# Performance work log

Hardware: AMD Instinct MI355X
Metric: run time of the kernel (lower is better)

The kernel has to match this reference:

```python
import jax, jax.numpy as jnp
import numpy as np


def _gru_scan(x, m, d, Wih, Whh, bih, bhh):
    # Returns pre-update hidden at each step (hiddens.append(hidden) BEFORE rnn_cell)
    H = Whh.shape[1]
    B = x.shape[0]
    h0 = jnp.zeros((B, H), x.dtype)
    xs = (jnp.swapaxes(x, 0, 1), jnp.swapaxes(m, 0, 1), jnp.swapaxes(d, 0, 1))  # [T,B,V]

    def step(h, inp):
        xt, mt, dt = inp
        gi = jnp.concatenate([xt, mt, dt], axis=1) @ Wih.T + bih  # [B,3H]
        gh = h @ Whh.T + bhh
        ir, iz, inn = jnp.split(gi, 3, axis=1)
        hr, hz, hn = jnp.split(gh, 3, axis=1)
        r = jax.nn.sigmoid(ir + hr)
        z = jax.nn.sigmoid(iz + hz)
        n = jnp.tanh(inn + r * hn)
        h_new = (1.0 - z) * n + z * h
        return h_new, h

    _, hs = jax.lax.scan(step, h0, xs)
    return jnp.swapaxes(hs, 0, 1)  # [B,T,H]


def setup_inputs() -> dict:
    key = jax.random.key(0)
    B, T, V, H = 512, 128, 59, 512
    ks = jax.random.split(key, 12)

    def u(k, shape, fan_in):
        s = 1.0 / np.sqrt(fan_in).astype(np.float32)
        return jax.random.uniform(k, shape, jnp.float32, -s, s)

    return {
        "values": jax.random.normal(ks[0], (B, T, V), jnp.float32),
        "masks": (jax.random.uniform(ks[1], (B, T, V)) < 0.8).astype(jnp.float32),
        "deltas_f": jax.random.uniform(ks[2], (B, T, V), jnp.float32),
        "deltas_b": jax.random.uniform(ks[3], (B, T, V), jnp.float32),
        # GRUCell(input=3V, hidden=H)
        "Wih": u(ks[4], (3 * H, 3 * V), 3 * V),
        "Whh": u(ks[5], (3 * H, H), H),
        "bih": jnp.zeros((3 * H,), jnp.float32),
        "bhh": jnp.zeros((3 * H,), jnp.float32),
        # hist_reg: Linear(2H -> V)
        "Wh": u(ks[6], (V, 2 * H), 2 * H),
        "bh": jnp.zeros((V,), jnp.float32),
        "Wf": u(ks[7], (V, V), V),
        "bf": jnp.zeros((V,), jnp.float32),
        # weight_combine: Linear(2V -> V)
        "Wc": u(ks[8], (V, 2 * V), 2 * V),
        "bc": jnp.zeros((V,), jnp.float32),
        # imputation: Linear(V -> V)
        "Wi": u(ks[9], (V, V), V),
        "bi": jnp.zeros((V,), jnp.float32),
    }


def reference(values, masks, deltas_f, deltas_b, Wih, Whh, bih, bhh,
              Wh, bh, Wf, bf, Wc, bc, Wi, bi):
    V = values.shape[-1]
    # forward-direction hiddens
    hf = _gru_scan(values, masks, deltas_f, Wih, Whh, bih, bhh)  # [B,T,H]
    # backward-direction: run GRU on time-flipped x/masks with deltas_b, then reverse list
    hb = _gru_scan(values[:, ::-1], masks[:, ::-1], deltas_b, Wih, Whh, bih, bhh)[:, ::-1]
    h = jnp.concatenate([hf, hb], axis=-1)  # [B,T,2H]
    x_v = h @ Wh.T + bh  # hist_reg
    mdiag = 1.0 - jnp.eye(V, dtype=values.dtype)
    x_u = values @ (Wf * mdiag).T + bf  # feat_reg
    x_h = x_u + jnp.concatenate([x_v, masks], axis=-1) @ Wc.T + bc
    imp = x_h @ Wi.T + bi
    # per-timestep masked MAE, summed over T (denominator is per-step mask count)
    num = jnp.sum(jnp.abs(values - imp) * masks, axis=(0, 2))  # [T]
    den = jnp.sum(masks, axis=(0, 2)) + 1e-5
    x_loss = jnp.sum(num / den)
    x_imp = masks * values + (1.0 - masks) * imp
    return x_imp, x_loss
```

## Files before the change

kernel.cpp:

```cpp
#include <hip/hip_runtime.h>
#include <stdint.h>


typedef unsigned short ushort_t;
typedef __bf16 bf16x8 __attribute__((ext_vector_type(8)));
typedef float f32x4 __attribute__((ext_vector_type(4)));
typedef unsigned int u32x4 __attribute__((ext_vector_type(4)));

__device__ __forceinline__ ushort_t f2bf(float f) {
    union { float f; uint32_t u; } c; c.f = f;
    uint32_t u = c.u;
    uint32_t r = (u + 0x7FFFu + ((u >> 16) & 1u)) >> 16;
    return (ushort_t)r;
}

__device__ __forceinline__ u32x4 load_b128_cached(const void* p) {
    u32x4 d;
    asm volatile("global_load_dwordx4 %0, %1, off" : "=v"(d) : "v"(p) : "memory");
    return d;
}
__device__ __forceinline__ u32x4 load_b128_mall(const void* p) {
    u32x4 d;
    asm volatile("global_load_dwordx4 %0, %1, off sc0 sc1" : "=v"(d) : "v"(p) : "memory");
    return d;
}
__device__ __forceinline__ void store_b16_mall(void* p, unsigned v) {
    asm volatile("global_store_short %0, %1, off sc0 sc1" :: "v"(p), "v"(v) : "memory");
}

__device__ __forceinline__ float fast_sigmoid(float x) {
    float e = __expf(-x);
    return __builtin_amdgcn_rcpf(1.f + e);
}
__device__ __forceinline__ float fast_tanh(float x) {
    float xc = fminf(fmaxf(x, -15.f), 15.f);
    float e = __expf(-2.f * xc);
    return (1.f - e) * __builtin_amdgcn_rcpf(1.f + e);
}

__global__ void prep_small(const float* __restrict__ Wih, const float* __restrict__ Whh,
                           const float* __restrict__ Wh,
                           const float* __restrict__ Wf, const float* __restrict__ bf_,
                           const float* __restrict__ Wc, const float* __restrict__ bc,
                           const float* __restrict__ Wi, const float* __restrict__ bi,
                           ushort_t* __restrict__ WhhB, ushort_t* __restrict__ WihB,
                           ushort_t* __restrict__ WhpB,
                           ushort_t* __restrict__ hf0, ushort_t* __restrict__ hb0,
                           float* __restrict__ hstate,
                           ushort_t* __restrict__ Wpost1, ushort_t* __restrict__ Wpost2,
                           float* __restrict__ bcP, float* __restrict__ biP,
                           unsigned* __restrict__ bar, float* __restrict__ outp)
{
    long long gid = (long long)blockIdx.x * blockDim.x + threadIdx.x;
    long long stride = (long long)gridDim.x * blockDim.x;

    if (gid == 0) outp[3866624] = 0.f;
    for (long long i = gid; i < 16 * 64; i += stride) bar[i] = 0u;
    for (long long i = gid; i < 1024LL * 512; i += stride) hstate[i] = 0.f;
    for (long long i = gid; i < 512LL * 512; i += stride) { hf0[i] = 0; hb0[i] = 0; }
    for (long long i = gid; i < 1536LL * 512; i += stride) WhhB[i] = f2bf(Whh[i]);
    for (long long i = gid; i < 1536LL * 192; i += stride) {
        int n = (int)(i / 192), c = (int)(i % 192);
        WihB[i] = (c < 177) ? f2bf(Wih[n * 177 + c]) : (ushort_t)0;
    }
    for (long long i = gid; i < 64LL * 1024; i += stride) {
        int n = (int)(i >> 10), k = (int)(i & 1023);
        WhpB[i] = (n < 59) ? f2bf(Wh[n * 1024 + k]) : (ushort_t)0;
    }
    for (long long i = gid; i < 64LL * 192; i += stride) {
        int n = (int)(i / 192), c = (int)(i % 192);
        float w = 0.f;
        if (n < 59) {
            if (c < 59)       w = (c == n) ? 0.f : Wf[n * 59 + c];
            else if (c < 118) w = Wc[n * 118 + (c - 59)];
            else if (c < 177) w = Wc[n * 118 + 59 + (c - 118)];
        }
        Wpost1[i] = f2bf(w);
    }
    for (long long i = gid; i < 64LL * 64; i += stride) {
        int n = (int)(i >> 6), k = (int)(i & 63);
        Wpost2[i] = (n < 59 && k < 59) ? f2bf(Wi[n * 59 + k]) : (ushort_t)0;
    }
    for (long long i = gid; i < 64; i += stride) {
        bcP[i] = (i < 59) ? (bf_[i] + bc[i]) : 0.f;
        biP[i] = (i < 59) ? bi[i] : 0.f;
    }
}

__global__ __launch_bounds__(192)
void prep_panels(const float* __restrict__ values, const float* __restrict__ masks,
                 const float* __restrict__ deltas_f, const float* __restrict__ deltas_b,
                 ushort_t* __restrict__ xcat_f, ushort_t* __restrict__ xcat_b,
                 ushort_t* __restrict__ pcat)
{
    const int row = blockIdx.x;
    const int c = threadIdx.x;
    const int b = row >> 7, t = row & 127;
    const int tr = 127 - t;
    const long long rowr = (long long)b * 128 + tr;

    float vf = 0.f;
    if (c < 59)       vf = values  [(long long)row * 59 + c];
    else if (c < 118) vf = masks   [(long long)row * 59 + (c - 59)];
    else if (c < 177) vf = deltas_f[(long long)row * 59 + (c - 118)];
    xcat_f[((size_t)t * 512 + b) * 192 + c] = (c < 177) ? f2bf(vf) : (ushort_t)0;

    float vb = 0.f;
    if (c < 59)       vb = values  [rowr * 59 + c];
    else if (c < 118) vb = masks   [rowr * 59 + (c - 59)];
    else if (c < 177) vb = deltas_b[(long long)row * 59 + (c - 118)];
    xcat_b[((size_t)t * 512 + b) * 192 + c] = (c < 177) ? f2bf(vb) : (ushort_t)0;

    if (c < 59)
        pcat[(size_t)row * 192 + c] = f2bf(values[(long long)row * 59 + c]);
    else if (c >= 118 && c < 177)
        pcat[(size_t)row * 192 + c] = f2bf(masks[(long long)row * 59 + (c - 118)]);
    else if (c >= 177)
        pcat[(size_t)row * 192 + c] = 0;
}

__global__ __launch_bounds__(512)
void recurrence_kernel(const ushort_t* __restrict__ WhhB, const ushort_t* __restrict__ WihB,
                       const float* __restrict__ bih, const float* __restrict__ bhh,
                       const ushort_t* __restrict__ xcat_f, const ushort_t* __restrict__ xcat_b,
                       ushort_t* __restrict__ hfS, ushort_t* __restrict__ hbS,
                       unsigned* __restrict__ bar)
{
    extern __shared__ char smem_c[];
    ushort_t* Bw = (ushort_t*)smem_c;
    ushort_t* As = Bw + 96 * 704;

    const int tid  = threadIdx.x;
    const int blk  = blockIdx.x;
    const int ublk = blk & 15;
    const int mblk = blk >> 4;
    const int u0   = ublk * 32;
    const bool fwd = (mblk < 8);
    const int rbase = (fwd ? mblk : mblk - 8) * 64;
    const ushort_t* xbase = fwd ? xcat_f : xcat_b;
    ushort_t* hS = fwd ? hfS : hbS;
    unsigned* gctr = bar + (unsigned)mblk * 64;

    for (int i = tid; i < 96 * 88; i += 512) {
        int row = i / 88, q = i - row * 88;
        int g = row >> 5, u = u0 + (row & 31);
        const ushort_t* src = (q < 64)
            ? WhhB + ((size_t)(g * 512 + u)) * 512 + q * 8
            : WihB + ((size_t)(g * 512 + u)) * 192 + (q - 64) * 8;
        int qs = q ^ (row & 7);
        *(u32x4*)&Bw[row * 704 + qs * 8] = *(const u32x4*)src;
    }

    const int lane = tid & 63, wv = tid >> 6;
    const int mt = wv >> 1, tc = wv & 1;
    const int l15 = lane & 15, lhi = lane >> 4;
    const int arow = tid >> 3, aj = tid & 7;
    const int awoff = arow * 64 + ((aj ^ (arow & 7)) * 8);
    const int aSw = l15 & 7;

    const int u = u0 + tc * 16 + l15;
    const float bR  = bih[u] + bhh[u];
    const float bZ  = bih[512 + u] + bhh[512 + u];
    const float bNX = bih[1024 + u];
    const float bNH = bhh[1024 + u];
    asm volatile("" :: "v"(bR), "v"(bZ), "v"(bNX), "v"(bNH));
    asm volatile("s_waitcnt vmcnt(0) lgkmcnt(0)" ::: "memory");
    __syncthreads();

    f32x4 hreg = {0.f, 0.f, 0.f, 0.f};
    f32x4 zero = {0.f, 0.f, 0.f, 0.f};
    u32x4 rx[3];
    u32x4 rh[5];

    auto mfma_pos = [&](int cbuf, int jBbase, f32x4& aR, f32x4& aZ, f32x4& accN) {
        const ushort_t* Ab = As + cbuf * 4096;
        #pragma unroll
        for (int ks = 0; ks < 64; ks += 32) {
            int j  = (ks >> 3) + lhi;
            int jB = jBbase + j;
            bf16x8 a  = *(const bf16x8*)&Ab[(mt * 16 + l15) * 64 + ((j ^ aSw) * 8)];
            bf16x8 b0 = *(const bf16x8*)&Bw[( 0 + tc * 16 + l15) * 704 + ((jB ^ aSw) * 8)];
            bf16x8 b1 = *(const bf16x8*)&Bw[(32 + tc * 16 + l15) * 704 + ((jB ^ aSw) * 8)];
            bf16x8 b2 = *(const bf16x8*)&Bw[(64 + tc * 16 + l15) * 704 + ((jB ^ aSw) * 8)];
            aR   = __builtin_amdgcn_mfma_f32_16x16x32_bf16(a, b0, aR, 0, 0, 0);
            aZ   = __builtin_amdgcn_mfma_f32_16x16x32_bf16(a, b1, aZ, 0, 0, 0);
            accN = __builtin_amdgcn_mfma_f32_16x16x32_bf16(a, b2, accN, 0, 0, 0);
        }
    };

    {
        const ushort_t* xr0 = xbase + (size_t)(rbase + arow) * 192 + aj * 8;
        rx[0] = load_b128_cached(xr0);
        rx[1] = load_b128_cached(xr0 + 64);
        rx[2] = load_b128_cached(xr0 + 128);
    }
    asm volatile("s_waitcnt vmcnt(0)" ::: "memory");

    for (int t = 0; t < 127; ++t) {
        const ushort_t* hrow = hS + (size_t)t * 262144 + (size_t)(rbase + arow) * 512 + aj * 8;
        ushort_t* hdst = hS + (size_t)(t + 1) * 262144;

        f32x4 accR = zero, accZ = zero, accNX = zero, accNH = zero;

        rh[0] = load_b128_mall(hrow);
        rh[1] = load_b128_mall(hrow + 64);
        rh[2] = load_b128_mall(hrow + 128);

        *(u32x4*)&As[awoff] = rx[0];
        __syncthreads();

        mfma_pos(0, 64, accR, accZ, accNX);
        rh[3] = load_b128_mall(hrow + 3 * 64);
        *(u32x4*)&As[4096 + awoff] = rx[1];
        __syncthreads();

        mfma_pos(1, 72, accR, accZ, accNX);
        rh[4] = load_b128_mall(hrow + 4 * 64);
        *(u32x4*)&As[awoff] = rx[2];
        {
            const ushort_t* xrn = xbase + (size_t)(t + 1) * 98304
                                + (size_t)(rbase + arow) * 192 + aj * 8;
            rx[0] = load_b128_cached(xrn);
            rx[1] = load_b128_cached(xrn + 64);
            rx[2] = load_b128_cached(xrn + 128);
        }
        __syncthreads();

        mfma_pos(0, 80, accR, accZ, accNX);
        asm volatile("s_waitcnt vmcnt(7)" ::: "memory");
        *(u32x4*)&As[4096 + awoff] = rh[0];
        rh[0] = load_b128_mall(hrow + 5 * 64);
        __syncthreads();

        mfma_pos(1, 0, accR, accZ, accNH);
        asm volatile("s_waitcnt vmcnt(7)" ::: "memory");
        *(u32x4*)&As[awoff] = rh[1];
        rh[1] = load_b128_mall(hrow + 6 * 64);
        __syncthreads();

        mfma_pos(0, 8, accR, accZ, accNH);
        asm volatile("s_waitcnt vmcnt(7)" ::: "memory");
        *(u32x4*)&As[4096 + awoff] = rh[2];
        rh[2] = load_b128_mall(hrow + 7 * 64);
        __syncthreads();

        mfma_pos(1, 16, accR, accZ, accNH);
        asm volatile("s_waitcnt vmcnt(7)" ::: "memory");
        *(u32x4*)&As[awoff] = rh[3];
        __syncthreads();

        mfma_pos(0, 24, accR, accZ, accNH);
        asm volatile("s_waitcnt vmcnt(6)" ::: "memory");
        *(u32x4*)&As[4096 + awoff] = rh[4];
        __syncthreads();

        mfma_pos(1, 32, accR, accZ, accNH);
        asm volatile("s_waitcnt vmcnt(2)" ::: "memory");
        *(u32x4*)&As[awoff] = rh[0];
        __syncthreads();

        mfma_pos(0, 40, accR, accZ, accNH);
        asm volatile("s_waitcnt vmcnt(1)" ::: "memory");
        *(u32x4*)&As[4096 + awoff] = rh[1];
        __syncthreads();

        mfma_pos(1, 48, accR, accZ, accNH);
        asm volatile("s_waitcnt vmcnt(0)" ::: "memory");
        *(u32x4*)&As[awoff] = rh[2];
        __syncthreads();

        mfma_pos(0, 56, accR, accZ, accNH);

        #pragma unroll
        for (int reg = 0; reg < 4; ++reg) {
            int m = rbase + mt * 16 + lhi * 4 + reg;
            float rr = fast_sigmoid(accR[reg] + bR);
            float zz = fast_sigmoid(accZ[reg] + bZ);
            float nn = fast_tanh(accNX[reg] + bNX + rr * (accNH[reg] + bNH));
            float hnew = (1.f - zz) * nn + zz * hreg[reg];
            hreg[reg] = hnew;
            store_b16_mall(hdst + (size_t)m * 512 + u, (unsigned)f2bf(hnew));
        }

        if (t < 126) {
            asm volatile("s_waitcnt vmcnt(0)" ::: "memory");
            __syncthreads();
            if (tid == 0) {
                atomicAdd(gctr, 1u);
                unsigned target = (unsigned)(t + 1) * 16u;
                while (__hip_atomic_load(gctr, __ATOMIC_RELAXED,
                                         __HIP_MEMORY_SCOPE_AGENT) < target)
                    __builtin_amdgcn_s_sleep(1);
            }
            __syncthreads();
        }
    }
}

__global__ __launch_bounds__(512)
void step_kernel(const ushort_t* __restrict__ hsrcF, const ushort_t* __restrict__ hsrcB,
                 ushort_t* __restrict__ hdstF, ushort_t* __restrict__ hdstB,
                 const ushort_t* __restrict__ xF, const ushort_t* __restrict__ xB,
                 const ushort_t* __restrict__ WhhB, const ushort_t* __restrict__ WihB,
                 const float* __restrict__ bih, const float* __restrict__ bhh,
                 float* __restrict__ hstate)
{
    __shared__ __align__(16) ushort_t As[64 * 64];
    __shared__ __align__(16) ushort_t Bs[96 * 64];

    const int tid  = threadIdx.x;
    const int ublk = blockIdx.x;
    const int mblk = blockIdx.y;
    const int u0   = ublk * 32;
    const bool fwd = (mblk < 8);
    const ushort_t* hsrc = fwd ? hsrcF : hsrcB;
    const ushort_t* xsrc = fwd ? xF : xB;
    ushort_t* hdst = fwd ? hdstF : hdstB;
    const int rbase = (fwd ? mblk : mblk - 8) * 64;

    const int lane = tid & 63, wv = tid >> 6;
    const int mt = wv >> 1, tc = wv & 1;
    const int l15 = lane & 15, lhi = lane >> 4;

    f32x4 zero = {0.f, 0.f, 0.f, 0.f};
    f32x4 accR = zero, accZ = zero, accNH = zero, accNX = zero;
    const int arow = tid >> 3, ac8 = (tid & 7) * 8;

    for (int chunk = 0; chunk < 11; ++chunk) {
        const bool ph1 = (chunk < 8);
        {
            const ushort_t* src = ph1
                ? hsrc + ((size_t)(rbase + arow)) * 512 + chunk * 64 + ac8
                : xsrc + ((size_t)(rbase + arow)) * 192 + (chunk - 8) * 64 + ac8;
            *(uint4*)&As[arow * 64 + ac8] = *(const uint4*)src;
        }
        {
            int rowB = tid >> 3; int c8 = (tid & 7) * 8;
            int g = rowB >> 5; int u = u0 + (rowB & 31);
            const ushort_t* src = ph1
                ? WhhB + ((size_t)(g * 512 + u)) * 512 + chunk * 64 + c8
                : WihB + ((size_t)(g * 512 + u)) * 192 + (chunk - 8) * 64 + c8;
            *(uint4*)&Bs[rowB * 64 + c8] = *(const uint4*)src;
            if (tid < 256) {
                int u2 = tid + 512;
                rowB = u2 >> 3; c8 = (u2 & 7) * 8;
                g = rowB >> 5; u = u0 + (rowB & 31);
                src = ph1
                    ? WhhB + ((size_t)(g * 512 + u)) * 512 + chunk * 64 + c8
                    : WihB + ((size_t)(g * 512 + u)) * 192 + (chunk - 8) * 64 + c8;
                *(uint4*)&Bs[rowB * 64 + c8] = *(const uint4*)src;
            }
        }
        __syncthreads();
        #pragma unroll
        for (int ks = 0; ks < 64; ks += 32) {
            bf16x8 a  = *(const bf16x8*)&As[(mt * 16 + l15) * 64 + ks + lhi * 8];
            bf16x8 b0 = *(const bf16x8*)&Bs[( 0 + tc * 16 + l15) * 64 + ks + lhi * 8];
            bf16x8 b1 = *(const bf16x8*)&Bs[(32 + tc * 16 + l15) * 64 + ks + lhi * 8];
            bf16x8 b2 = *(const bf16x8*)&Bs[(64 + tc * 16 + l15) * 64 + ks + lhi * 8];
            accR = __builtin_amdgcn_mfma_f32_16x16x32_bf16(a, b0, accR, 0, 0, 0);
            accZ = __builtin_amdgcn_mfma_f32_16x16x32_bf16(a, b1, accZ, 0, 0, 0);
            if (ph1) accNH = __builtin_amdgcn_mfma_f32_16x16x32_bf16(a, b2, accNH, 0, 0, 0);
            else     accNX = __builtin_amdgcn_mfma_f32_16x16x32_bf16(a, b2, accNX, 0, 0, 0);
        }
        __syncthreads();
    }

    const int u = u0 + tc * 16 + l15;
    const float bR  = bih[u] + bhh[u];
    const float bZ  = bih[512 + u] + bhh[512 + u];
    const float bNX = bih[1024 + u];
    const float bNH = bhh[1024 + u];
    #pragma unroll
    for (int reg = 0; reg < 4; ++reg) {
        int m = mblk * 64 + mt * 16 + lhi * 4 + reg;
        float r = 1.f / (1.f + __expf(-(accR[reg] + bR)));
        float z = 1.f / (1.f + __expf(-(accZ[reg] + bZ)));
        float n = tanhf(accNX[reg] + bNX + r * (accNH[reg] + bNH));
        size_t idx = (size_t)m * 512 + u;
        float hold = hstate[idx];
        float hnew = (1.f - z) * n + z * hold;
        hstate[idx] = hnew;
        size_t bloc = (size_t)(fwd ? m : m - 512) * 512 + u;
        hdst[bloc] = f2bf(hnew);
    }
}

__global__ __launch_bounds__(256)
void xv_kernel(const ushort_t* __restrict__ hf, const ushort_t* __restrict__ hb,
               const ushort_t* __restrict__ WhpB, const float* __restrict__ bh,
               ushort_t* __restrict__ pcat)
{
    __shared__ __align__(16) ushort_t As[128 * 64];
    __shared__ __align__(16) ushort_t Bs[64 * 64];
    const int b = blockIdx.x;
    const int tid = threadIdx.x;
    const int lane = tid & 63, wv = tid >> 6;
    const int l15 = lane & 15, lhi = lane >> 4;

    f32x4 zero = {0.f, 0.f, 0.f, 0.f};
    f32x4 acc[2][4];
    #pragma unroll
    for (int i = 0; i < 2; ++i)
        #pragma unroll
        for (int j = 0; j < 4; ++j) acc[i][j] = zero;

    for (int chunk = 0; chunk < 16; ++chunk) {
        const bool fw = (chunk < 8);
        #pragma unroll
        for (int s = 0; s < 4; ++s) {
            int unit = tid + s * 256;
            int row = unit >> 3;
            int c8 = (unit & 7) * 8;
            const ushort_t* src = fw
                ? hf + ((size_t)row * 512 + b) * 512 + chunk * 64 + c8
                : hb + ((size_t)(127 - row) * 512 + b) * 512 + (chunk - 8) * 64 + c8;
            *(uint4*)&As[row * 64 + c8] = *(const uint4*)src;
        }
        #pragma unroll
        for (int s = 0; s < 2; ++s) {
            int unit = tid + s * 256;
            int row = unit >> 3;
            int c8 = (unit & 7) * 8;
            *(uint4*)&Bs[row * 64 + c8] =
                *(const uint4*)(WhpB + (size_t)row * 1024 + chunk * 64 + c8);
        }
        __syncthreads();
        #pragma unroll
        for (int ks = 0; ks < 64; ks += 32) {
            bf16x8 bfr[4];
            #pragma unroll
            for (int nt = 0; nt < 4; ++nt)
                bfr[nt] = *(const bf16x8*)&Bs[(nt * 16 + l15) * 64 + ks + lhi * 8];
            #pragma unroll
            for (int mt2 = 0; mt2 < 2; ++mt2) {
                bf16x8 a = *(const bf16x8*)&As[(wv * 32 + mt2 * 16 + l15) * 64 + ks + lhi * 8];
                #pragma unroll
                for (int nt = 0; nt < 4; ++nt)
                    acc[mt2][nt] = __builtin_amdgcn_mfma_f32_16x16x32_bf16(a, bfr[nt], acc[mt2][nt], 0, 0, 0);
            }
        }
        __syncthreads();
    }
    #pragma unroll
    for (int mt2 = 0; mt2 < 2; ++mt2) {
        #pragma unroll
        for (int nt = 0; nt < 4; ++nt) {
            int col = nt * 16 + l15;
            if (col < 59) {
                float bhc = bh[col];
                #pragma unroll
                for (int reg = 0; reg < 4; ++reg) {
                    int t = wv * 32 + mt2 * 16 + lhi * 4 + reg;
                    pcat[((size_t)b * 128 + t) * 192 + 59 + col] = f2bf(acc[mt2][nt][reg] + bhc);
                }
            }
        }
    }
}

__global__ __launch_bounds__(256)
void post_kernel(const ushort_t* __restrict__ pcat,
                 const ushort_t* __restrict__ Wpost1, const ushort_t* __restrict__ Wpost2,
                 const float* __restrict__ bcP, const float* __restrict__ biP,
                 const float* __restrict__ values, const float* __restrict__ masks,
                 float* __restrict__ out, float* __restrict__ pnum, float* __restrict__ pden)
{
    __shared__ __align__(16) ushort_t A1[64 * 200];
    __shared__ __align__(16) ushort_t B1[64 * 200];
    __shared__ __align__(16) ushort_t B2[64 * 72];

    const int tid = threadIdx.x;
    const int blk = blockIdx.x;
    const int lane = tid & 63, wv = tid >> 6;
    const int l15 = lane & 15, lhi = lane >> 4;

    #pragma unroll
    for (int s = 0; s < 6; ++s) {
        int unit = tid + s * 256;
        int row = unit / 24, c8 = (unit % 24) * 8;
        *(uint4*)&A1[row * 200 + c8] =
            *(const uint4*)(pcat + ((size_t)blk * 64 + row) * 192 + c8);
        *(uint4*)&B1[row * 200 + c8] =
            *(const uint4*)(Wpost1 + (size_t)row * 192 + c8);
    }
    #pragma unroll
    for (int s = 0; s < 2; ++s) {
        int unit = tid + s * 256;
        int row = unit >> 3, c8 = (unit & 7) * 8;
        *(uint4*)&B2[row * 72 + c8] = *(const uint4*)(Wpost2 + (size_t)row * 64 + c8);
    }
    __syncthreads();

    f32x4 zero = {0.f, 0.f, 0.f, 0.f};
    f32x4 acc1[4];
    #pragma unroll
    for (int nt = 0; nt < 4; ++nt) acc1[nt] = zero;

    #pragma unroll
    for (int ks = 0; ks < 192; ks += 32) {
        bf16x8 a = *(const bf16x8*)&A1[(wv * 16 + l15) * 200 + ks + lhi * 8];
        #pragma unroll
        for (int nt = 0; nt < 4; ++nt) {
            bf16x8 bb = *(const bf16x8*)&B1[(nt * 16 + l15) * 200 + ks + lhi * 8];
            acc1[nt] = __builtin_amdgcn_mfma_f32_16x16x32_bf16(a, bb, acc1[nt], 0, 0, 0);
        }
    }
    __syncthreads();

    #pragma unroll
    for (int nt = 0; nt < 4; ++nt) {
        int col = nt * 16 + l15;
        float bcv = bcP[col];
        #pragma unroll
        for (int reg = 0; reg < 4; ++reg) {
            int row = wv * 16 + lhi * 4 + reg;
            A1[row * 72 + col] = f2bf(acc1[nt][reg] + bcv);
        }
    }
    __syncthreads();

    f32x4 acc2[4];
    #pragma unroll
    for (int nt = 0; nt < 4; ++nt) acc2[nt] = zero;
    #pragma unroll
    for (int ks = 0; ks < 64; ks += 32) {
        bf16x8 a = *(const bf16x8*)&A1[(wv * 16 + l15) * 72 + ks + lhi * 8];
        #pragma unroll
        for (int nt = 0; nt < 4; ++nt) {
            bf16x8 bb = *(const bf16x8*)&B2[(nt * 16 + l15) * 72 + ks + lhi * 8];
            acc2[nt] = __builtin_amdgcn_mfma_f32_16x16x32_bf16(a, bb, acc2[nt], 0, 0, 0);
        }
    }

    float biR[4];
    #pragma unroll
    for (int nt = 0; nt < 4; ++nt) biR[nt] = biP[nt * 16 + l15];

    #pragma unroll
    for (int reg = 0; reg < 4; ++reg) {
        size_t rowg = (size_t)blk * 64 + wv * 16 + lhi * 4 + reg;
        float esum = 0.f, dsum = 0.f;
        #pragma unroll
        for (int nt = 0; nt < 4; ++nt) {
            int col = nt * 16 + l15;
            if (col < 59) {
                float imp = acc2[nt][reg] + biR[nt];
                float v = values[rowg * 59 + col];
                float m = masks [rowg * 59 + col];
                out[rowg * 59 + col] = m * v + (1.f - m) * imp;
                esum += fabsf(v - imp) * m;
                dsum += m;
            }
        }
        #pragma unroll
        for (int o = 1; o < 16; o <<= 1) {
            esum += __shfl_xor(esum, o);
            dsum += __shfl_xor(dsum, o);
        }
        if (l15 == 0) { pnum[rowg] = esum; pden[rowg] = dsum; }
    }
}

__global__ __launch_bounds__(256)
void loss_kernel(const float* __restrict__ pnum, const float* __restrict__ pden,
                 float* __restrict__ out)
{
    __shared__ float sn[4], sd[4];
    const int t = blockIdx.x;
    const int tid = threadIdx.x;
    float a = 0.f, b = 0.f;
    for (int bb = tid; bb < 512; bb += 256) {
        a += pnum[(size_t)bb * 128 + t];
        b += pden[(size_t)bb * 128 + t];
    }
    #pragma unroll
    for (int o = 32; o >= 1; o >>= 1) {
        a += __shfl_xor(a, o);
        b += __shfl_xor(b, o);
    }
    const int wv = tid >> 6;
    if ((tid & 63) == 0) { sn[wv] = a; sd[wv] = b; }
    __syncthreads();
    if (tid == 0) {
        float A = sn[0] + sn[1] + sn[2] + sn[3];
        float B = sd[0] + sd[1] + sd[2] + sd[3];
        atomicAdd(out + 3866624, A / (B + 1e-5f));
    }
}

extern "C" void kernel_launch(void* const* d_in, const int* in_sizes, int n_in,
                              void* d_out, int out_size, void* d_ws, size_t ws_size,
                              hipStream_t stream)
{
    const float* values   = (const float*)d_in[0];
    const float* masks    = (const float*)d_in[1];
    const float* deltas_f = (const float*)d_in[2];
    const float* deltas_b = (const float*)d_in[3];
    const float* Wih = (const float*)d_in[4];
    const float* Whh = (const float*)d_in[5];
    const float* bih = (const float*)d_in[6];
    const float* bhh = (const float*)d_in[7];
    const float* Wh  = (const float*)d_in[8];
    const float* bh  = (const float*)d_in[9];
    const float* Wf  = (const float*)d_in[10];
    const float* bf_ = (const float*)d_in[11];
    const float* Wc  = (const float*)d_in[12];
    const float* bc  = (const float*)d_in[13];
    const float* Wi  = (const float*)d_in[14];
    const float* bi  = (const float*)d_in[15];
    float* out = (float*)d_out;

    uint8_t* ws = (uint8_t*)d_ws;
    size_t off = 0;
    auto alloc = [&](size_t bytes) -> void* {
        void* p = ws + off;
        off = (off + bytes + 255) & ~((size_t)255);
        return p;
    };
    ushort_t* xcat_f = (ushort_t*)alloc(128ULL * 512 * 192 * 2);
    ushort_t* xcat_b = (ushort_t*)alloc(128ULL * 512 * 192 * 2);
    ushort_t* WhhB   = (ushort_t*)alloc(1536ULL * 512 * 2);
    ushort_t* WihB   = (ushort_t*)alloc(1536ULL * 192 * 2);
    ushort_t* WhpB   = (ushort_t*)alloc(64ULL * 1024 * 2);
    ushort_t* hfS    = (ushort_t*)alloc(128ULL * 512 * 512 * 2);
    ushort_t* hbS    = (ushort_t*)alloc(128ULL * 512 * 512 * 2);
    float*    hstate = (float*)alloc(1024ULL * 512 * 4);
    ushort_t* pcat   = (ushort_t*)alloc(65536ULL * 192 * 2);
    ushort_t* Wpost1 = (ushort_t*)alloc(64ULL * 192 * 2);
    ushort_t* Wpost2 = (ushort_t*)alloc(64ULL * 64 * 2);
    float*    bcP    = (float*)alloc(64 * 4);
    float*    biP    = (float*)alloc(64 * 4);
    float*    pnum   = (float*)alloc(65536ULL * 4);
    float*    pden   = (float*)alloc(65536ULL * 4);
    unsigned* bar    = (unsigned*)alloc(16 * 64 * 4);

    prep_small<<<1024, 256, 0, stream>>>(Wih, Whh, Wh, Wf, bf_, Wc, bc, Wi, bi,
                                         WhhB, WihB, WhpB, hfS, hbS, hstate,
                                         Wpost1, Wpost2, bcP, biP, bar, out);
    prep_panels<<<65536, 192, 0, stream>>>(values, masks, deltas_f, deltas_b,
                                           xcat_f, xcat_b, pcat);

    const unsigned smemBytes = (96u * 704u + 2u * 64u * 64u) * 2u;
    hipError_t aerr = hipFuncSetAttribute((const void*)recurrence_kernel,
                                          hipFuncAttributeMaxDynamicSharedMemorySize,
                                          (int)smemBytes);
    hipError_t lerr = hipErrorUnknown;
    if (aerr == hipSuccess) {
        const ushort_t* a0 = WhhB; const ushort_t* a1 = WihB;
        const float* a2 = bih; const float* a3 = bhh;
        const ushort_t* a4 = xcat_f; const ushort_t* a5 = xcat_b;
        ushort_t* a6 = hfS; ushort_t* a7 = hbS;
        unsigned* a8 = bar;
        void* args[] = { &a0, &a1, &a2, &a3, &a4, &a5, &a6, &a7, &a8 };
        lerr = hipLaunchCooperativeKernel((const void*)recurrence_kernel,
                                          dim3(256), dim3(512), args, smemBytes, stream);
    }
    if (lerr != hipSuccess) {
        for (int t = 0; t < 127; ++t) {
            step_kernel<<<dim3(16, 16), 512, 0, stream>>>(
                hfS + (size_t)t * 512 * 512, hbS + (size_t)t * 512 * 512,
                hfS + (size_t)(t + 1) * 512 * 512, hbS + (size_t)(t + 1) * 512 * 512,
                xcat_f + (size_t)t * 512 * 192, xcat_b + (size_t)t * 512 * 192,
                WhhB, WihB, bih, bhh, hstate);
        }
    }

    xv_kernel<<<512, 256, 0, stream>>>(hfS, hbS, WhpB, bh, pcat);
    post_kernel<<<1024, 256, 0, stream>>>(pcat, Wpost1, Wpost2, bcP, biP,
                                          values, masks, out, pnum, pden);
    loss_kernel<<<128, 256, 0, stream>>>(pnum, pden, out);
}
```

Baseline: 840.4 us.

## Replace atomic-counter grid barrier with per-block flag slots polled by one wave

```diff
diff --git a/kernel.cpp b/kernel.cpp
--- a/kernel.cpp
+++ b/kernel.cpp
@@ -19,13 +19,16 @@
     asm volatile("global_load_dwordx4 %0, %1, off" : "=v"(d) : "v"(p) : "memory");
     return d;
 }
-__device__ __forceinline__ u32x4 load_b128_mall(const void* p) {
+__device__ __forceinline__ u32x4 load_b128_l2(const void* p) {
     u32x4 d;
-    asm volatile("global_load_dwordx4 %0, %1, off sc0 sc1" : "=v"(d) : "v"(p) : "memory");
+    asm volatile("global_load_dwordx4 %0, %1, off sc0" : "=v"(d) : "v"(p) : "memory");
     return d;
 }
 __device__ __forceinline__ void store_b16_mall(void* p, unsigned v) {
     asm volatile("global_store_short %0, %1, off sc0 sc1" :: "v"(p), "v"(v) : "memory");
+}
+__device__ __forceinline__ void store_u32_mall(void* p, unsigned v) {
+    asm volatile("global_store_dword %0, %1, off sc0 sc1" :: "v"(p), "v"(v) : "memory");
 }
 
 __device__ __forceinline__ float fast_sigmoid(float x) {
@@ -55,7 +58,7 @@
     long long stride = (long long)gridDim.x * blockDim.x;
 
     if (gid == 0) outp[3866624] = 0.f;
-    for (long long i = gid; i < 16 * 64; i += stride) bar[i] = 0u;
+    for (long long i = gid; i < 16LL * 16 * 32; i += stride) bar[i] = 0u;
     for (long long i = gid; i < 1024LL * 512; i += stride) hstate[i] = 0.f;
     for (long long i = gid; i < 512LL * 512; i += stride) { hf0[i] = 0; hb0[i] = 0; }
     for (long long i = gid; i < 1536LL * 512; i += stride) WhhB[i] = f2bf(Whh[i]);
@@ -139,7 +142,6 @@
     const int rbase = (fwd ? mblk : mblk - 8) * 64;
     const ushort_t* xbase = fwd ? xcat_f : xcat_b;
     ushort_t* hS = fwd ? hfS : hbS;
-    unsigned* gctr = bar + (unsigned)mblk * 64;
 
     for (int i = tid; i < 96 * 88; i += 512) {
         int row = i / 88, q = i - row * 88;
@@ -157,6 +159,9 @@
     const int arow = tid >> 3, aj = tid & 7;
     const int awoff = arow * 64 + ((aj ^ (arow & 7)) * 8);
     const int aSw = l15 & 7;
+
+    unsigned* myslot = bar + ((size_t)(mblk * 16 + ublk)) * 32;
+    const unsigned* pollp = bar + ((size_t)(mblk * 16 + (lane & 15))) * 32;
 
     const int u = u0 + tc * 16 + l15;
     const float bR  = bih[u] + bhh[u];
@@ -202,20 +207,20 @@
 
         f32x4 accR = zero, accZ = zero, accNX = zero, accNH = zero;
 
-        rh[0] = load_b128_mall(hrow);
-        rh[1] = load_b128_mall(hrow + 64);
-        rh[2] = load_b128_mall(hrow + 128);
+        rh[0] = load_b128_l2(hrow);
+        rh[1] = load_b128_l2(hrow + 64);
+        rh[2] = load_b128_l2(hrow + 128);
 
         *(u32x4*)&As[awoff] = rx[0];
         __syncthreads();
 
         mfma_pos(0, 64, accR, accZ, accNX);
-        rh[3] = load_b128_mall(hrow + 3 * 64);
+        rh[3] = load_b128_l2(hrow + 3 * 64);
         *(u32x4*)&As[4096 + awoff] = rx[1];
         __syncthreads();
 
         mfma_pos(1, 72, accR, accZ, accNX);
-        rh[4] = load_b128_mall(hrow + 4 * 64);
+        rh[4] = load_b128_l2(hrow + 4 * 64);
         *(u32x4*)&As[awoff] = rx[2];
         {
             const ushort_t* xrn = xbase + (size_t)(t + 1) * 98304
@@ -229,19 +234,19 @@
         mfma_pos(0, 80, accR, accZ, accNX);
         asm volatile("s_waitcnt vmcnt(7)" ::: "memory");
         *(u32x4*)&As[4096 + awoff] = rh[0];
-        rh[0] = load_b128_mall(hrow + 5 * 64);
+        rh[0] = load_b128_l2(hrow + 5 * 64);
         __syncthreads();
 
         mfma_pos(1, 0, accR, accZ, accNH);
         asm volatile("s_waitcnt vmcnt(7)" ::: "memory");
         *(u32x4*)&As[awoff] = rh[1];
-        rh[1] = load_b128_mall(hrow + 6 * 64);
+        rh[1] = load_b128_l2(hrow + 6 * 64);
         __syncthreads();
 
         mfma_pos(0, 8, accR, accZ, accNH);
         asm volatile("s_waitcnt vmcnt(7)" ::: "memory");
         *(u32x4*)&As[4096 + awoff] = rh[2];
-        rh[2] = load_b128_mall(hrow + 7 * 64);
+        rh[2] = load_b128_l2(hrow + 7 * 64);
         __syncthreads();
 
         mfma_pos(1, 16, accR, accZ, accNH);
@@ -285,12 +290,21 @@
         if (t < 126) {
             asm volatile("s_waitcnt vmcnt(0)" ::: "memory");
             __syncthreads();
-            if (tid == 0) {
-                atomicAdd(gctr, 1u);
-                unsigned target = (unsigned)(t + 1) * 16u;
-                while (__hip_atomic_load(gctr, __ATOMIC_RELAXED,
-                                         __HIP_MEMORY_SCOPE_AGENT) < target)
+            if (tid == 0) store_u32_mall(myslot, (unsigned)(t + 1));
+            if (wv == 0) {
+                const unsigned target = (unsigned)(t + 1);
+                const bool need = (lane < 16) && (lane != ublk);
+                for (;;) {
+                    unsigned v = 0;
+                    if (need) {
+                        asm volatile("global_load_dword %0, %1, off sc0 sc1"
+                                     : "=v"(v) : "v"(pollp) : "memory");
+                    }
+                    asm volatile("s_waitcnt vmcnt(0)" ::: "memory");
+                    bool ok = need ? (v >= target) : true;
+                    if (__ballot(ok) == ~0ULL) break;
                     __builtin_amdgcn_s_sleep(1);
+                }
             }
             __syncthreads();
         }
@@ -633,7 +647,7 @@
     float*    biP    = (float*)alloc(64 * 4);
     float*    pnum   = (float*)alloc(65536ULL * 4);
     float*    pden   = (float*)alloc(65536ULL * 4);
-    unsigned* bar    = (unsigned*)alloc(16 * 64 * 4);
+    unsigned* bar    = (unsigned*)alloc(16ULL * 16 * 32 * 4);
 
     prep_small<<<1024, 256, 0, stream>>>(Wih, Whh, Wh, Wf, bf_, Wc, bc, Wi, bi,
                                          WhhB, WihB, WhpB, hfS, hbS, hstate,
```

Measured after the change: 796.6 us. -5.2%, faster.
